# Optimization experiments

Hardware: AMD Instinct MI355X
Metric: run time of the kernel (lower is better)

Reference implementation:

```python
import jax, jax.numpy as jnp
import numpy as np

N = 2048          # num_nodes
A = 100           # anchor count (hard-coded in _select_anchor_points)


def setup_inputs() -> dict:
    key = jax.random.key(0)
    k1, k2, k3 = jax.random.split(key, 3)
    motifGraph = jax.random.uniform(k1, (N, N), dtype=jnp.float32)
    node_weights = jax.random.uniform(k2, (N,), dtype=jnp.float32)
    weight_matrix = jax.random.uniform(k3, (N, A), dtype=jnp.float32)
    sigma = jnp.array(1.0, dtype=jnp.float32)
    return {"motifGraph": motifGraph, "node_weights": node_weights,
            "weight_matrix": weight_matrix, "sigma": sigma}


def _floyd_warshall(w):
    # w: [n,n] edge-weight matrix (inf = no edge, 0 on diagonal)
    n = w.shape[0]
    def step(d, k):
        # d_ij = min(d_ij, d_ik + d_kj)
        d = jnp.minimum(d, d[:, k][:, None] + d[k, :][None, :])
        return d, None
    d, _ = jax.lax.scan(step, w, jnp.arange(n))
    return d


def reference(motifGraph, node_weights, weight_matrix, sigma):
    n = motifGraph.shape[0]
    # _adjust_motif_graph: row-scale by node weights. The original detaches
    # before the scipy floyd_warshall call, so no grad flows through it.
    adj = jax.lax.stop_gradient(motifGraph * node_weights[:n, None])
    # csr_matrix semantics: zero entries are "no edge"; directed=False takes
    # the min of w_ij and w_ji; diagonal distance is 0.
    w = jnp.where(adj > 0, adj, jnp.inf)
    w = jnp.minimum(w, w.T)
    idx = jnp.arange(n)
    w = w.at[idx, idx].set(0.0)
    dist = _floyd_warshall(w)
    dist = jnp.where(jnp.isinf(dist), 100.0, dist)
    # _select_anchor_points: top-100 node weights (all indices < n here)
    anchors = jnp.argsort(-jax.lax.stop_gradient(node_weights))[:A]
    consensus_vectors = dist[:, anchors]                      # [n, A]
    distance_sums = (consensus_vectors.sum(axis=1) - 100.0).sum() / (n * A)
    weighted = weight_matrix[:n, :] * consensus_vectors       # [n, A]
    # build_consensus_graph: cdist(...)**4 == (squared euclidean dist)**2
    xx = jnp.sum(weighted * weighted, axis=1)                 # [n]
    sq = jnp.maximum(xx[:, None] + xx[None, :] - 2.0 * weighted @ weighted.T, 0.0)
    consensus_graph = jnp.exp(-(sq * sq) / (2.0 * sigma ** 2))
    return consensus_vectors, distance_sums, consensus_graph
```

## Files before the change

kernel.cpp:

```cpp
#include <hip/hip_runtime.h>
#include <stdint.h>

#define NN 2048
#define AA 100
#define NT 32

#define F_DIAG   256
#define F_ROW    512
#define F_COL    1536
#define F_PREROW 2560
#define F_PRECOL 2624

typedef float floatx4 __attribute__((ext_vector_type(4)));

template<bool AL> __device__ __forceinline__ float4 ld4(const float* __restrict__ p) {
  if (AL) return *(const float4*)p;
  return make_float4(p[0], p[1], p[2], p[3]);
}
template<bool AL> __device__ __forceinline__ void st4(float* __restrict__ p, float4 v) {
  if (AL) { *(float4*)p = v; }
  else { p[0] = v.x; p[1] = v.y; p[2] = v.z; p[3] = v.w; }
}

__device__ __forceinline__ void minplus16(const float (*A)[68], const float (*B)[68],
                                          float c[4][4], int i0, int j0) {
#pragma unroll 4
  for (int k4 = 0; k4 < 16; ++k4) {
    const int k = k4 * 4;
    float4 a0 = *(const float4*)&A[i0 + 0][k];
    float4 a1 = *(const float4*)&A[i0 + 1][k];
    float4 a2 = *(const float4*)&A[i0 + 2][k];
    float4 a3 = *(const float4*)&A[i0 + 3][k];
    float4 b0 = *(const float4*)&B[k + 0][j0];
    float4 b1 = *(const float4*)&B[k + 1][j0];
    float4 b2 = *(const float4*)&B[k + 2][j0];
    float4 b3 = *(const float4*)&B[k + 3][j0];
#define MP1(ii, jj, f)                                                           \
    c[ii][jj] = fminf(fminf(fminf(fminf(c[ii][jj], a##ii.x + b0.f),              \
                                  a##ii.y + b1.f),                               \
                            a##ii.z + b2.f),                                     \
                      a##ii.w + b3.f)
#define MP_ROW(ii) MP1(ii, 0, x); MP1(ii, 1, y); MP1(ii, 2, z); MP1(ii, 3, w)
    MP_ROW(0); MP_ROW(1); MP_ROW(2); MP_ROW(3);
#undef MP_ROW
#undef MP1
  }
}

__device__ __forceinline__ void close_seq(float (*S)[68], float c[4][4],
                                          int i0, int j0, int ty, int tx) {
  for (int kb = 0; kb < 16; ++kb) {
#pragma unroll
    for (int h = 0; h < 2; ++h) {
      const int k = kb * 4 + h * 2;
      float4 br  = *(const float4*)&S[k][j0];
      float4 br2 = *(const float4*)&S[k + 1][j0];
      float dkk1 = S[k][k + 1];
      float dk1k = S[k + 1][k];
      float a0 = S[i0 + 0][k],     a1 = S[i0 + 1][k],
            a2 = S[i0 + 2][k],     a3 = S[i0 + 3][k];
      float e0 = S[i0 + 0][k + 1], e1 = S[i0 + 1][k + 1],
            e2 = S[i0 + 2][k + 1], e3 = S[i0 + 3][k + 1];
      float4 brp;
      brp.x = fminf(br2.x, dk1k + br.x);
      brp.y = fminf(br2.y, dk1k + br.y);
      brp.z = fminf(br2.z, dk1k + br.z);
      brp.w = fminf(br2.w, dk1k + br.w);
      e0 = fminf(e0, a0 + dkk1);
      e1 = fminf(e1, a1 + dkk1);
      e2 = fminf(e2, a2 + dkk1);
      e3 = fminf(e3, a3 + dkk1);
#define CS2(ii, aa, ee)                                                     \
      c[ii][0] = fminf(fminf(c[ii][0], aa + br.x), ee + brp.x);             \
      c[ii][1] = fminf(fminf(c[ii][1], aa + br.y), ee + brp.y);             \
      c[ii][2] = fminf(fminf(c[ii][2], aa + br.z), ee + brp.z);             \
      c[ii][3] = fminf(fminf(c[ii][3], aa + br.w), ee + brp.w)
      CS2(0, a0, e0); CS2(1, a1, e1); CS2(2, a2, e2); CS2(3, a3, e3);
#undef CS2
      const int kn = k + 2;
      if (kn < 64) {
        const int ow = kn >> 2;
        const int ri = (h == 0) ? 2 : 0;
        if (ow == ty) {
          *(float4*)&S[kn][j0] =
              make_float4(c[ri][0], c[ri][1], c[ri][2], c[ri][3]);
          *(float4*)&S[kn + 1][j0] =
              make_float4(c[ri + 1][0], c[ri + 1][1], c[ri + 1][2], c[ri + 1][3]);
        }
        if (ow == tx) {
          S[i0 + 0][kn] = c[0][ri]; S[i0 + 0][kn + 1] = c[0][ri + 1];
          S[i0 + 1][kn] = c[1][ri]; S[i0 + 1][kn + 1] = c[1][ri + 1];
          S[i0 + 2][kn] = c[2][ri]; S[i0 + 2][kn + 1] = c[2][ri + 1];
          S[i0 + 3][kn] = c[3][ri]; S[i0 + 3][kn + 1] = c[3][ri + 1];
        }
      }
      __syncthreads();
    }
  }
}

template<int LAZY>
__device__ __forceinline__ void waitflag(int* f) {
  int it = 0;
  while (__hip_atomic_load(f, __ATOMIC_RELAXED, __HIP_MEMORY_SCOPE_AGENT) == 0) {
    if (++it > 24) __builtin_amdgcn_s_sleep(LAZY);
  }
}
__device__ __forceinline__ void setflag(int* f) {
  __hip_atomic_store(f, 1, __ATOMIC_RELAXED, __HIP_MEMORY_SCOPE_AGENT);
}

__device__ __forceinline__ void stage64(const float* __restrict__ g,
                                        float (*S)[68], int t) {
#pragma unroll
  for (int l = 0; l < 4; ++l) {
    int idx = l * 256 + t;
    int row = idx >> 4, c4 = (idx & 15) * 4;
    *(float4*)&S[row][c4] = *(const float4*)&g[row * 64 + c4];
  }
}
__device__ __forceinline__ void pub64_wt(float* __restrict__ g,
                                         const float c[4][4], int i0, int j0) {
#pragma unroll
  for (int ii = 0; ii < 4; ++ii) {
    floatx4 v = {c[ii][0], c[ii][1], c[ii][2], c[ii][3]};
    float* p = &g[(i0 + ii) * 64 + j0];
    asm volatile("global_store_dwordx4 %0, %1, off sc0 sc1"
                 :: "v"(p), "v"(v) : "memory");
  }
  asm volatile("s_waitcnt vmcnt(0)" ::: "memory");
}

__global__ __launch_bounds__(256, 4) void fw_persist(
    const float* __restrict__ mg, const float* __restrict__ nw,
    float* __restrict__ dist, int* __restrict__ Wi,
    float* __restrict__ diagb, float* __restrict__ rowb,
    float* __restrict__ colb, float* __restrict__ prerow,
    float* __restrict__ precol) {
  __shared__ __align__(16) float As[64][68];
  __shared__ __align__(16) float Bs[64][68];
  const int bx = blockIdx.x, by = blockIdx.y;
  const int t = threadIdx.x;
  const int tx = t & 15, ty = t >> 4;
  const int i0 = ty * 4, j0 = tx * 4;
  int* DIAGF   = Wi + F_DIAG;
  int* ROWF    = Wi + F_ROW;
  int* COLF    = Wi + F_COL;
  int* PREROWF = Wi + F_PREROW;
  int* PRECOLF = Wi + F_PRECOL;

#pragma unroll
  for (int l = 0; l < 4; ++l) {
    int idx = l * 256 + t;
    int r = idx >> 4, c4 = (idx & 15) * 4;
    float4 g = *(const float4*)&mg[(bx * 64 + r) * NN + by * 64 + c4];
    Bs[c4 + 0][r] = g.x; Bs[c4 + 1][r] = g.y;
    Bs[c4 + 2][r] = g.z; Bs[c4 + 3][r] = g.w;
  }
  __syncthreads();
  float c[4][4];
  {
    float4 nwj = *(const float4*)&nw[bx * 64 + j0];
#pragma unroll
    for (int ii = 0; ii < 4; ++ii) {
      int rl = i0 + ii;
      int i = by * 64 + rl;
      float nwi = nw[i];
      float4 m = *(const float4*)&mg[i * NN + bx * 64 + j0];
      float4 bt = *(const float4*)&Bs[rl][j0];
      float av[4] = {m.x * nwi, m.y * nwi, m.z * nwi, m.w * nwi};
      float bv[4] = {bt.x * nwj.x, bt.y * nwj.y, bt.z * nwj.z, bt.w * nwj.w};
#pragma unroll
      for (int q = 0; q < 4; ++q) {
        float wa = av[q] > 0.0f ? av[q] : __builtin_huge_valf();
        float wb = bv[q] > 0.0f ? bv[q] : __builtin_huge_valf();
        float v = fminf(wa, wb);
        if (i == bx * 64 + j0 + q) v = 0.0f;
        c[ii][q] = v;
      }
    }
  }
  if ((by == 0 && bx == 1) || (by == 1 && bx == 0)) {
    pub64_wt((by == 0) ? prerow : precol, c, i0, j0);
    __syncthreads();
    if (t == 0) setflag((by == 0) ? PREROWF + 0 : PRECOLF + 0);
  }
  if (bx == 0 && by == 0) {
    __syncthreads();
#pragma unroll
    for (int ii = 0; ii < 4; ++ii)
      *(float4*)&As[i0 + ii][j0] = make_float4(c[ii][0], c[ii][1], c[ii][2], c[ii][3]);
    __syncthreads();
    close_seq(As, c, i0, j0, ty, tx);
    pub64_wt(diagb, c, i0, j0);
    __syncthreads();
    if (t == 0) setflag(DIAGF + 0);
  }

  for (int r = 0; r < NT; ++r) {
    const bool crit = (by == r) || (bx == r) || (by == r + 1) || (bx == r + 1);
    if (crit) __builtin_amdgcn_s_setprio(1);
    else      __builtin_amdgcn_s_setprio(0);
    if (by == r && bx == r) continue;
    const bool closer = (bx == r + 1) && (by == r + 1) && (r + 1 < NT);
    if (closer) {
      if (t == 0) {
        waitflag<1>(DIAGF + r);
        waitflag<1>(PREROWF + r);
        waitflag<1>(PRECOLF + r);
      }
      __syncthreads();
      stage64(precol + r * 4096, As, t);
      stage64(diagb + r * 4096, Bs, t);
      __syncthreads();
      float cp[4][4], rp[4][4];
#pragma unroll
      for (int ii = 0; ii < 4; ++ii) {
        float4 q = *(const float4*)&As[i0 + ii][j0];
        cp[ii][0] = q.x; cp[ii][1] = q.y; cp[ii][2] = q.z; cp[ii][3] = q.w;
      }
      minplus16(As, Bs, cp, i0, j0);
      __syncthreads();
      stage64(prerow + r * 4096, As, t);
      __syncthreads();
#pragma unroll
      for (int ii = 0; ii < 4; ++ii) {
        float4 q = *(const float4*)&As[i0 + ii][j0];
        rp[ii][0] = q.x; rp[ii][1] = q.y; rp[ii][2] = q.z; rp[ii][3] = q.w;
      }
      minplus16(Bs, As, rp, i0, j0);
      __syncthreads();
#pragma unroll
      for (int ii = 0; ii < 4; ++ii) {
        *(float4*)&As[i0 + ii][j0] = make_float4(cp[ii][0], cp[ii][1], cp[ii][2], cp[ii][3]);
        *(float4*)&Bs[i0 + ii][j0] = make_float4(rp[ii][0], rp[ii][1], rp[ii][2], rp[ii][3]);
      }
      __syncthreads();
      minplus16(As, Bs, c, i0, j0);
      __syncthreads();
#pragma unroll
      for (int ii = 0; ii < 4; ++ii)
        *(float4*)&As[i0 + ii][j0] = make_float4(c[ii][0], c[ii][1], c[ii][2], c[ii][3]);
      __syncthreads();
      close_seq(As, c, i0, j0, ty, tx);
      pub64_wt(diagb + (r + 1) * 4096, c, i0, j0);
      __syncthreads();
      if (t == 0) setflag(DIAGF + r + 1);
    } else if (by == r || bx == r) {
      const bool isRow = (by == r);
      __syncthreads();
      float (*Ow)[68] = isRow ? Bs : As;
#pragma unroll
      for (int ii = 0; ii < 4; ++ii)
        *(float4*)&Ow[i0 + ii][j0] =
            make_float4(c[ii][0], c[ii][1], c[ii][2], c[ii][3]);
      if (t == 0) waitflag<1>(DIAGF + r);
      __syncthreads();
      stage64(diagb + r * 4096, isRow ? As : Bs, t);
      __syncthreads();
      minplus16(As, Bs, c, i0, j0);
      float* ob = isRow ? rowb + (r * NT + bx) * 4096
                        : colb + (by * NT + r) * 4096;
      pub64_wt(ob, c, i0, j0);
      __syncthreads();
      if (t == 0) setflag(isRow ? ROWF + r * NT + bx : COLF + by * NT + r);
    } else {
      if (t == 0) {
        if (crit) {
          waitflag<1>(ROWF + r * NT + bx);
          waitflag<1>(COLF + by * NT + r);
        } else {
          waitflag<8>(ROWF + r * NT + bx);
          waitflag<8>(COLF + by * NT + r);
        }
      }
      __syncthreads();
      stage64(colb + (by * NT + r) * 4096, As, t);
      stage64(rowb + (r * NT + bx) * 4096, Bs, t);
      __syncthreads();
      minplus16(As, Bs, c, i0, j0);
      if (r + 2 < NT) {
        if (by == r + 1 && bx == r + 2) {
          pub64_wt(prerow + (r + 1) * 4096, c, i0, j0);
          __syncthreads();
          if (t == 0) setflag(PREROWF + r + 1);
        } else if (by == r + 2 && bx == r + 1) {
          pub64_wt(precol + (r + 1) * 4096, c, i0, j0);
          __syncthreads();
          if (t == 0) setflag(PRECOLF + r + 1);
        }
      }
    }
  }
  __builtin_amdgcn_s_setprio(0);

  float* ob = &dist[(by * 64) * NN + bx * 64];
#pragma unroll
  for (int ii = 0; ii < 4; ++ii)
    *(float4*)&ob[(i0 + ii) * NN + j0] =
        make_float4(c[ii][0], c[ii][1], c[ii][2], c[ii][3]);
}

template<bool AL>
__global__ __launch_bounds__(256) void build_w_kernel(
    const float* __restrict__ mg, const float* __restrict__ nw,
    float* __restrict__ w) {
  __shared__ float Tt[64][65];
  __shared__ __align__(16) float As[64][68];
  int bi = blockIdx.y, bj = blockIdx.x;
  int t = threadIdx.x;
  const bool diag0 = (bi == 0) && (bj == 0);
#pragma unroll
  for (int l = 0; l < 4; ++l) {
    int idx = l * 256 + t;
    int r = idx >> 4, c4 = (idx & 15) * 4;
    float4 g = *(const float4*)&mg[(bj * 64 + r) * NN + bi * 64 + c4];
    Tt[c4 + 0][r] = g.x; Tt[c4 + 1][r] = g.y;
    Tt[c4 + 2][r] = g.z; Tt[c4 + 3][r] = g.w;
  }
  __syncthreads();
#pragma unroll
  for (int l = 0; l < 4; ++l) {
    int idx = l * 256 + t;
    int r = idx >> 4, c4 = (idx & 15) * 4;
    int i = bi * 64 + r, j = bj * 64 + c4;
    float4 m = *(const float4*)&mg[i * NN + j];
    float4 nwj = *(const float4*)&nw[j];
    float nwi = nw[i];
    float av[4] = {m.x * nwi, m.y * nwi, m.z * nwi, m.w * nwi};
    float bv[4] = {Tt[r][c4 + 0] * nwj.x, Tt[r][c4 + 1] * nwj.y,
                   Tt[r][c4 + 2] * nwj.z, Tt[r][c4 + 3] * nwj.w};
    float vv[4];
#pragma unroll
    for (int q = 0; q < 4; ++q) {
      float wa = av[q] > 0.0f ? av[q] : __builtin_huge_valf();
      float wb = bv[q] > 0.0f ? bv[q] : __builtin_huge_valf();
      float v = fminf(wa, wb);
      if (i == j + q) v = 0.0f;
      vv[q] = v;
    }
    float4 v4 = make_float4(vv[0], vv[1], vv[2], vv[3]);
    if (diag0) {
      *(float4*)&As[r][c4] = v4;
    } else {
      st4<AL>(&w[i * NN + j], v4);
    }
  }
  if (diag0) {
    __syncthreads();
    int tx = t & 15, ty = t >> 4;
    int i0 = ty * 4, j0 = tx * 4;
    float c[4][4];
#pragma unroll
    for (int ii = 0; ii < 4; ++ii) {
      float4 q = *(const float4*)&As[i0 + ii][j0];
      c[ii][0] = q.x; c[ii][1] = q.y; c[ii][2] = q.z; c[ii][3] = q.w;
    }
    close_seq(As, c, i0, j0, ty, tx);
#pragma unroll
    for (int ii = 0; ii < 4; ++ii)
      st4<AL>(&w[(i0 + ii) * NN + j0],
              make_float4(c[ii][0], c[ii][1], c[ii][2], c[ii][3]));
  }
}

template<bool AL>
__global__ __launch_bounds__(256) void fw_p2(float* __restrict__ d, int r) {
  __shared__ __align__(16) float As[64][68];
  __shared__ __align__(16) float Bs[64][68];
  int tile = blockIdx.x, side = blockIdx.y;
  if (tile == r) return;
  int t = threadIdx.x;
  int dbase = (r * 64) * NN + r * 64;
  int obase = (side == 0) ? (r * 64) * NN + tile * 64
                          : (tile * 64) * NN + r * 64;
  float (*Da)[68] = (side == 0) ? As : Bs;
  float (*Ow)[68] = (side == 0) ? Bs : As;
#pragma unroll
  for (int l = 0; l < 4; ++l) {
    int idx = l * 256 + t;
    int row = idx >> 4, c4 = (idx & 15) * 4;
    *(float4*)&Da[row][c4] = ld4<AL>(&d[dbase + row * NN + c4]);
    *(float4*)&Ow[row][c4] = ld4<AL>(&d[obase + row * NN + c4]);
  }
  int tx = t & 15, ty = t >> 4;
  int i0 = ty * 4, j0 = tx * 4;
  __syncthreads();
  float c[4][4];
#pragma unroll
  for (int ii = 0; ii < 4; ++ii) {
    float4 q = *(const float4*)&Ow[i0 + ii][j0];
    c[ii][0] = q.x; c[ii][1] = q.y; c[ii][2] = q.z; c[ii][3] = q.w;
  }
  minplus16(As, Bs, c, i0, j0);
#pragma unroll
  for (int ii = 0; ii < 4; ++ii)
    st4<AL>(&d[obase + (i0 + ii) * NN + j0],
            make_float4(c[ii][0], c[ii][1], c[ii][2], c[ii][3]));
}

template<bool AL>
__global__ __launch_bounds__(256) void fw_p3(float* __restrict__ d, int r) {
  __shared__ __align__(16) float As[64][68];
  __shared__ __align__(16) float Bs[64][68];
  int bx = blockIdx.x, by = blockIdx.y;
  if (bx == r || by == r) return;
  int t = threadIdx.x;
#pragma unroll
  for (int l = 0; l < 4; ++l) {
    int idx = l * 256 + t;
    int row = idx >> 4, c4 = (idx & 15) * 4;
    *(float4*)&As[row][c4] = ld4<AL>(&d[(by * 64 + row) * NN + r * 64 + c4]);
    *(float4*)&Bs[row][c4] = ld4<AL>(&d[(r * 64 + row) * NN + bx * 64 + c4]);
  }
  int tx = t & 15, ty = t >> 4;
  int i0 = ty * 4, j0 = tx * 4;
  int obase = (by * 64) * NN + bx * 64;
  float c[4][4];
#pragma unroll
  for (int ii = 0; ii < 4; ++ii) {
    float4 q = ld4<AL>(&d[obase + (i0 + ii) * NN + j0]);
    c[ii][0] = q.x; c[ii][1] = q.y; c[ii][2] = q.z; c[ii][3] = q.w;
  }
  __syncthreads();
  minplus16(As, Bs, c, i0, j0);

  bool closer = (bx == r + 1) && (by == r + 1) && (r + 1 < NT);
  if (closer) {
    __syncthreads();
#pragma unroll
    for (int ii = 0; ii < 4; ++ii)
      *(float4*)&As[i0 + ii][j0] = make_float4(c[ii][0], c[ii][1], c[ii][2], c[ii][3]);
    __syncthreads();
    close_seq(As, c, i0, j0, ty, tx);
  }
#pragma unroll
  for (int ii = 0; ii < 4; ++ii)
    st4<AL>(&d[obase + (i0 + ii) * NN + j0],
            make_float4(c[ii][0], c[ii][1], c[ii][2], c[ii][3]));
}

__global__ __launch_bounds__(256) void anchors_kernel(
    const float* __restrict__ nw, int* __restrict__ anchors) {
  __shared__ __align__(16) float s[NN];
  int t = threadIdx.x;
#pragma unroll
  for (int l = 0; l < NN / 256; ++l) s[l * 256 + t] = nw[l * 256 + t];
  __syncthreads();
  int i = blockIdx.x * 64 + (t >> 2);
  int q = t & 3;
  float wi = s[i];
  int rank = 0;
  int jb = q * (NN / 4);
  for (int j = jb; j < jb + NN / 4; j += 4) {
    float4 v = *(const float4*)&s[j];
    rank += (int)(v.x > wi) + ((int)(v.x == wi) & (int)(j + 0 < i));
    rank += (int)(v.y > wi) + ((int)(v.y == wi) & (int)(j + 1 < i));
    rank += (int)(v.z > wi) + ((int)(v.z == wi) & (int)(j + 2 < i));
    rank += (int)(v.w > wi) + ((int)(v.w == wi) & (int)(j + 3 < i));
  }
  rank += __shfl_xor(rank, 1);
  rank += __shfl_xor(rank, 2);
  if (q == 0 && rank < AA) anchors[rank] = i;
}

__global__ __launch_bounds__(256) void cv_kernel(
    const float* __restrict__ dist, const int* __restrict__ anchors,
    float* __restrict__ cv_out, float* __restrict__ sum_acc) {
  int idx = blockIdx.x * 256 + threadIdx.x;
  int i = idx / 100, a = idx - i * 100;
  float dv = dist[i * NN + anchors[a]];
  if (isinf(dv)) dv = 100.0f;
  cv_out[idx] = dv;
  float v = dv;
#pragma unroll
  for (int off = 32; off > 0; off >>= 1) v += __shfl_down(v, off);
  __shared__ float sv[4];
  int lane = threadIdx.x & 63, w = threadIdx.x >> 6;
  if (lane == 0) sv[w] = v;
  __syncthreads();
  if (threadIdx.x == 0) atomicAdd(sum_acc, sv[0] + sv[1] + sv[2] + sv[3]);
}

__global__ __launch_bounds__(256) void graph_kernel(
    const float* __restrict__ wm, const float* __restrict__ cv,
    const float* __restrict__ sigma, float* __restrict__ graph) {
  __shared__ __align__(16) float As[64][108];
  __shared__ __align__(16) float Bs[64][108];
  __shared__ float xs[64], ys[64];
  int bx = blockIdx.x, by = blockIdx.y;
  int t = threadIdx.x;
#pragma unroll
  for (int l = 0; l < 7; ++l) {
    int idx = l * 256 + t;
    if (idx < 1600) {
      int row = idx / 25, c4 = (idx - row * 25) * 4;
      float4 wa = *(const float4*)&wm[(by * 64 + row) * AA + c4];
      float4 ca = *(const float4*)&cv[(by * 64 + row) * AA + c4];
      *(float4*)&As[row][c4] =
          make_float4(wa.x * ca.x, wa.y * ca.y, wa.z * ca.z, wa.w * ca.w);
      float4 wb = *(const float4*)&wm[(bx * 64 + row) * AA + c4];
      float4 cb = *(const float4*)&cv[(bx * 64 + row) * AA + c4];
      *(float4*)&Bs[row][c4] =
          make_float4(wb.x * cb.x, wb.y * cb.y, wb.z * cb.z, wb.w * cb.w);
    }
  }
  __syncthreads();
  if (t < 64) {
    float s = 0.0f;
    for (int k4 = 0; k4 < 25; ++k4) {
      float4 q = *(const float4*)&As[t][k4 * 4];
      s += q.x * q.x + q.y * q.y + q.z * q.z + q.w * q.w;
    }
    xs[t] = s;
  } else if (t < 128) {
    int r = t - 64;
    float s = 0.0f;
    for (int k4 = 0; k4 < 25; ++k4) {
      float4 q = *(const float4*)&Bs[r][k4 * 4];
      s += q.x * q.x + q.y * q.y + q.z * q.z + q.w * q.w;
    }
    ys[r] = s;
  }
  __syncthreads();
  int tx = t & 15, ty = t >> 4;
  float acc[4][4] = {{0.0f}};
#pragma unroll 5
  for (int k4 = 0; k4 < 25; ++k4) {
    int k = k4 * 4;
    float4 a_[4], b_[4];
#pragma unroll
    for (int ii = 0; ii < 4; ++ii) a_[ii] = *(const float4*)&As[ty + 16 * ii][k];
#pragma unroll
    for (int jj = 0; jj < 4; ++jj) b_[jj] = *(const float4*)&Bs[tx + 16 * jj][k];
#pragma unroll
    for (int ii = 0; ii < 4; ++ii)
#pragma unroll
      for (int jj = 0; jj < 4; ++jj)
        acc[ii][jj] += a_[ii].x * b_[jj].x + a_[ii].y * b_[jj].y +
                       a_[ii].z * b_[jj].z + a_[ii].w * b_[jj].w;
  }
  float s = *sigma;
  float inv2s2 = 0.5f / (s * s);
#pragma unroll
  for (int ii = 0; ii < 4; ++ii) {
    int gi = by * 64 + ty + 16 * ii;
    float xi = xs[ty + 16 * ii];
#pragma unroll
    for (int jj = 0; jj < 4; ++jj) {
      int gj = bx * 64 + tx + 16 * jj;
      float sq = fmaxf(xi + ys[tx + 16 * jj] - 2.0f * acc[ii][jj], 0.0f);
      graph[gi * NN + gj] = __expf(-(sq * sq) * inv2s2);
    }
  }
}

__global__ void finalize_kernel(const float* __restrict__ sum_acc,
                                float* __restrict__ out) {
  if (threadIdx.x == 0)
    *out = (*sum_acc - 204800.0f) / 204800.0f;
}

template<bool AL>
static void run_fw_fallback(const float* mg, const float* nw, float* dist,
                            hipStream_t stream) {
  build_w_kernel<AL><<<dim3(NT, NT), 256, 0, stream>>>(mg, nw, dist);
  for (int r = 0; r < NT; ++r) {
    fw_p2<AL><<<dim3(NT, 2), 256, 0, stream>>>(dist, r);
    fw_p3<AL><<<dim3(NT, NT), 256, 0, stream>>>(dist, r);
  }
}

static bool coop_ok() {
  static int ok = -1;
  if (ok < 0) {
    int dev = 0;
    (void)hipGetDevice(&dev);
    int coopAttr = 0;
    (void)hipDeviceGetAttribute(&coopAttr, hipDeviceAttributeCooperativeLaunch, dev);
    int cus = 0;
    (void)hipDeviceGetAttribute(&cus, hipDeviceAttributeMultiprocessorCount, dev);
    int nb = 0;
    hipError_t e = hipOccupancyMaxActiveBlocksPerMultiprocessor(&nb, fw_persist, 256, 0);
    ok = (e == hipSuccess && coopAttr && nb > 0 && (long)nb * cus >= NT * NT) ? 1 : 0;
  }
  return ok == 1;
}

extern "C" void kernel_launch(void* const* d_in, const int* in_sizes, int n_in,
                              void* d_out, int out_size, void* d_ws, size_t ws_size,
                              hipStream_t stream) {
  (void)in_sizes; (void)n_in; (void)out_size;
  const float* mg    = (const float*)d_in[0];
  const float* nw    = (const float*)d_in[1];
  const float* wm    = (const float*)d_in[2];
  const float* sigma = (const float*)d_in[3];
  float* out        = (float*)d_out;
  float* cv_out     = out;
  float* scalar_out = out + 204800;
  float* graph_out  = out + 204801;

  float* W = (float*)d_ws;
  float* sum_acc = W;
  int* anchors   = (int*)(W + 4);
  const size_t needP = (size_t)(16384 + (size_t)NN * NN + 3 * NT * 4096 +
                                2 * (size_t)NT * NT * 4096) * sizeof(float);
  const bool bigP  = ws_size >= needP;
  const bool bigF  = ws_size >= (size_t)(2048 + (size_t)NN * NN) * sizeof(float);
  float* dist = bigP ? (W + 16384) : (bigF ? (W + 2048) : graph_out);
  const bool al = ((((uintptr_t)dist) & 15) == 0);

  (void)hipMemsetAsync(W, 0, 16384, stream);

  bool launched = false;
  if (bigP && al && coop_ok()) {
    int* Wi = (int*)W;
    float* diagb  = dist + (size_t)NN * NN;
    float* rowb   = diagb + NT * 4096;
    float* colb   = rowb + (size_t)NT * NT * 4096;
    float* prerow = colb + (size_t)NT * NT * 4096;
    float* precol = prerow + NT * 4096;
    void* args[] = {(void*)&mg, (void*)&nw, (void*)&dist, (void*)&Wi,
                    (void*)&diagb, (void*)&rowb, (void*)&colb,
                    (void*)&prerow, (void*)&precol};
    hipError_t ce = hipLaunchCooperativeKernel(fw_persist, dim3(NT, NT),
                                               dim3(256, 1, 1), args, 0, stream);
    launched = (ce == hipSuccess);
  }
  if (!launched) {
    if (al) run_fw_fallback<true>(mg, nw, dist, stream);
    else    run_fw_fallback<false>(mg, nw, dist, stream);
  }

  anchors_kernel<<<NN / 64, 256, 0, stream>>>(nw, anchors);
  cv_kernel<<<800, 256, 0, stream>>>(dist, anchors, cv_out, sum_acc);
  graph_kernel<<<dim3(NT, NT), 256, 0, stream>>>(wm, cv_out, sigma, graph_out);
  finalize_kernel<<<1, 64, 0, stream>>>(sum_acc, scalar_out);
}
```

Measured before the change: 951.1 us.

## Shorten diagonal-closer critical path and tier spin-wait backoff by proximity

The next-diagonal closer block now does one fewer min-plus pass. It computes the row panel update first, then combines the column panel with it directly, which removes one staging round trip and a sync on the critical path. Flag waits become tiered: the pivot row/column blocks and the two corner blocks that feed the closer spin with no sleep. Blocks near the pivot sleep briefly, and distant blocks sleep longer to reduce memory-polling contention. The closer also polls all three flags in a single loop. The risk is that busy-spinning without sleep steals issue slots from co-resident work.

```diff
diff --git a/kernel.cpp b/kernel.cpp
--- a/kernel.cpp
+++ b/kernel.cpp
@@ -101,9 +101,11 @@
 
 template<int LAZY>
 __device__ __forceinline__ void waitflag(int* f) {
-  int it = 0;
-  while (__hip_atomic_load(f, __ATOMIC_RELAXED, __HIP_MEMORY_SCOPE_AGENT) == 0) {
-    if (++it > 24) __builtin_amdgcn_s_sleep(LAZY);
+  if (LAZY == 0) {
+    while (__hip_atomic_load(f, __ATOMIC_RELAXED, __HIP_MEMORY_SCOPE_AGENT) == 0) {}
+  } else {
+    while (__hip_atomic_load(f, __ATOMIC_RELAXED, __HIP_MEMORY_SCOPE_AGENT) == 0)
+      __builtin_amdgcn_s_sleep(LAZY);
   }
 }
 __device__ __forceinline__ void setflag(int* f) {
@@ -124,7 +126,7 @@
 #pragma unroll
   for (int ii = 0; ii < 4; ++ii) {
     floatx4 v = {c[ii][0], c[ii][1], c[ii][2], c[ii][3]};
-    float* p = &g[(i0 + ii) * 64 + j0];
+    float* p = &g[(ii + i0) * 64 + j0];
     asm volatile("global_store_dwordx4 %0, %1, off sc0 sc1"
                  :: "v"(p), "v"(v) : "memory");
   }
@@ -205,36 +207,29 @@
     const bool closer = (bx == r + 1) && (by == r + 1) && (r + 1 < NT);
     if (closer) {
       if (t == 0) {
-        waitflag<1>(DIAGF + r);
-        waitflag<1>(PREROWF + r);
-        waitflag<1>(PRECOLF + r);
+        while (__hip_atomic_load(DIAGF + r, __ATOMIC_RELAXED,
+                                 __HIP_MEMORY_SCOPE_AGENT) == 0 ||
+               __hip_atomic_load(PREROWF + r, __ATOMIC_RELAXED,
+                                 __HIP_MEMORY_SCOPE_AGENT) == 0 ||
+               __hip_atomic_load(PRECOLF + r, __ATOMIC_RELAXED,
+                                 __HIP_MEMORY_SCOPE_AGENT) == 0) {}
       }
       __syncthreads();
-      stage64(precol + r * 4096, As, t);
-      stage64(diagb + r * 4096, Bs, t);
-      __syncthreads();
-      float cp[4][4], rp[4][4];
+      stage64(diagb + r * 4096, As, t);
+      stage64(prerow + r * 4096, Bs, t);
+      __syncthreads();
+      float rp[4][4];
 #pragma unroll
       for (int ii = 0; ii < 4; ++ii) {
-        float4 q = *(const float4*)&As[i0 + ii][j0];
-        cp[ii][0] = q.x; cp[ii][1] = q.y; cp[ii][2] = q.z; cp[ii][3] = q.w;
-      }
-      minplus16(As, Bs, cp, i0, j0);
-      __syncthreads();
-      stage64(prerow + r * 4096, As, t);
-      __syncthreads();
-#pragma unroll
-      for (int ii = 0; ii < 4; ++ii) {
-        float4 q = *(const float4*)&As[i0 + ii][j0];
+        float4 q = *(const float4*)&Bs[i0 + ii][j0];
         rp[ii][0] = q.x; rp[ii][1] = q.y; rp[ii][2] = q.z; rp[ii][3] = q.w;
       }
-      minplus16(Bs, As, rp, i0, j0);
-      __syncthreads();
-#pragma unroll
-      for (int ii = 0; ii < 4; ++ii) {
-        *(float4*)&As[i0 + ii][j0] = make_float4(cp[ii][0], cp[ii][1], cp[ii][2], cp[ii][3]);
+      minplus16(As, Bs, rp, i0, j0);
+      __syncthreads();
+      stage64(precol + r * 4096, As, t);
+#pragma unroll
+      for (int ii = 0; ii < 4; ++ii)
         *(float4*)&Bs[i0 + ii][j0] = make_float4(rp[ii][0], rp[ii][1], rp[ii][2], rp[ii][3]);
-      }
       __syncthreads();
       minplus16(As, Bs, c, i0, j0);
       __syncthreads();
@@ -254,7 +249,7 @@
       for (int ii = 0; ii < 4; ++ii)
         *(float4*)&Ow[i0 + ii][j0] =
             make_float4(c[ii][0], c[ii][1], c[ii][2], c[ii][3]);
-      if (t == 0) waitflag<1>(DIAGF + r);
+      if (t == 0) waitflag<0>(DIAGF + r);
       __syncthreads();
       stage64(diagb + r * 4096, isRow ? As : Bs, t);
       __syncthreads();
@@ -265,13 +260,19 @@
       __syncthreads();
       if (t == 0) setflag(isRow ? ROWF + r * NT + bx : COLF + by * NT + r);
     } else {
+      const bool corner = (r + 2 < NT) &&
+          ((by == r + 1 && bx == r + 2) || (by == r + 2 && bx == r + 1));
+      const bool near = (by <= r + 2) || (bx <= r + 2);
       if (t == 0) {
-        if (crit) {
-          waitflag<1>(ROWF + r * NT + bx);
-          waitflag<1>(COLF + by * NT + r);
-        } else {
+        if (corner) {
+          waitflag<0>(ROWF + r * NT + bx);
+          waitflag<0>(COLF + by * NT + r);
+        } else if (near) {
           waitflag<8>(ROWF + r * NT + bx);
           waitflag<8>(COLF + by * NT + r);
+        } else {
+          waitflag<64>(ROWF + r * NT + bx);
+          waitflag<64>(COLF + by * NT + r);
         }
       }
       __syncthreads();
@@ -279,16 +280,11 @@
       stage64(rowb + (r * NT + bx) * 4096, Bs, t);
       __syncthreads();
       minplus16(As, Bs, c, i0, j0);
-      if (r + 2 < NT) {
-        if (by == r + 1 && bx == r + 2) {
-          pub64_wt(prerow + (r + 1) * 4096, c, i0, j0);
-          __syncthreads();
-          if (t == 0) setflag(PREROWF + r + 1);
-        } else if (by == r + 2 && bx == r + 1) {
-          pub64_wt(precol + (r + 1) * 4096, c, i0, j0);
-          __syncthreads();
-          if (t == 0) setflag(PRECOLF + r + 1);
-        }
+      if (corner) {
+        const bool isRowC = (by == r + 1);
+        pub64_wt((isRowC ? prerow : precol) + (r + 1) * 4096, c, i0, j0);
+        __syncthreads();
+        if (t == 0) setflag((isRowC ? PREROWF : PRECOLF) + r + 1);
       }
     }
   }
```

After: 922.3 us. 3.0% less time.
